# Kernel tuning notes

Hardware: AMD Instinct MI355X
Metric: run time of the kernel (lower is better)

## Reference

```python
import jax, jax.numpy as jnp
import numpy as np

MARGIN = 1.0
N, D = 8192, 128
NUM_CLASSES = 1024


def setup_inputs() -> dict:
    key = jax.random.key(0)
    k1, k2, k3 = jax.random.split(key, 3)
    a = jax.random.normal(k1, (N, D), dtype=jnp.float32)
    b = jax.random.normal(k2, (N, D), dtype=jnp.float32)
    # L2-normalize embeddings (standard for metric learning; keeps exp() stable)
    a = a / jnp.linalg.norm(a, axis=1, keepdims=True)
    b = b / jnp.linalg.norm(b, axis=1, keepdims=True)
    labels = jax.random.randint(k3, (N,), 0, NUM_CLASSES, dtype=jnp.int64 if jax.config.jax_enable_x64 else jnp.int32)
    return {"a": a, "b": b, "labels": labels}


def reference(a, b, labels):
    # S[i, j] = a_i . b_j  -- full pairwise similarity, one GEMM
    S = a @ b.T  # [N, N]
    same = labels[:, None] == labels[None, :]  # [N, N]
    eye = jnp.eye(labels.shape[0], dtype=bool)
    pos_mask = same & ~eye          # ordered positive pairs (i != j, same label)
    neg_mask = ~same                # ordered negative pairs (labels differ)
    # V[i] = sum_k in neg(i) exp(margin + S[i, k])
    V = jnp.sum(jnp.where(neg_mask, jnp.exp(MARGIN + S), 0.0), axis=1)  # [N]
    # per positive pair (i, j): max(log(V_i + V_j) - S_ij, 0)^2
    hinge = jnp.maximum(jnp.log(V[:, None] + V[None, :]) - S, 0.0)
    comp = jnp.where(pos_mask, hinge * hinge, 0.0)
    num_pos = jnp.sum(pos_mask)
    loss = jnp.sum(comp) / (2.0 * num_pos.astype(S.dtype))
    return loss
```

## Files before the change

### kernel.cpp

```cpp
#include <hip/hip_runtime.h>

#define NN 8192
#define DD 128
#define MAXCLS 64
#define NCHUNK 8
#define LOG2E 1.4426950408889634f
#define E1    2.718281828459045f

typedef __attribute__((ext_vector_type(8))) short bf16x8;
typedef __attribute__((ext_vector_type(4))) float f32x4;

#if __has_builtin(__builtin_amdgcn_exp2f)
#define EXP2F(x) __builtin_amdgcn_exp2f(x)
#else
#define EXP2F(x) exp2f(x)
#endif

__device__ __forceinline__ void load16_lds(const unsigned short* g, unsigned short* l) {
    __builtin_amdgcn_global_load_lds(
        (const __attribute__((address_space(1))) unsigned int*)g,
        (__attribute__((address_space(3))) unsigned int*)l,
        16, 0, 0);
}

__device__ __forceinline__ unsigned short f2bf(float x) {
    unsigned u = __float_as_uint(x);
    u = (u + 0x7FFFu + ((u >> 16) & 1u)) >> 16;
    return (unsigned short)u;
}

__global__ __launch_bounds__(256) void ml_convert_kernel(
    const float* __restrict__ a, const float* __restrict__ b,
    const int* __restrict__ labels,
    unsigned short* __restrict__ abf, unsigned short* __restrict__ bbf,
    int* __restrict__ cnt, int* __restrict__ list)
{
    int t = blockIdx.x * 256 + threadIdx.x;
    const float* src = a;
    unsigned short* dst = abf;
    int idx = t;
    float scale = LOG2E;
    if (t >= 262144) { src = b; dst = bbf; idx = t - 262144; scale = 1.0f; }
    float4 v = ((const float4*)src)[idx];
    ushort4 o;
    o.x = f2bf(v.x * scale); o.y = f2bf(v.y * scale);
    o.z = f2bf(v.z * scale); o.w = f2bf(v.w * scale);
    ((ushort4*)dst)[idx] = o;

    if (t < NN) {
        int c = labels[t];
        int p = atomicAdd(&cnt[c], 1);
        if (p < MAXCLS) list[c * MAXCLS + p] = t;
    }
}

__global__ __launch_bounds__(256, 2) void ml_vsum_gemm_kernel(
    const unsigned short* __restrict__ abf, const unsigned short* __restrict__ bbf,
    float* __restrict__ Vp)
{
    __shared__ unsigned short As[128 * DD];
    __shared__ unsigned short Bs[2][64 * DD];
    __shared__ float red[2][64];

    const int tid  = threadIdx.x;
    const int lane = tid & 63;
    const int wv   = tid >> 6;
    const int row0 = blockIdx.y * 128;
    const int j0   = blockIdx.x * 1024;

    const int lr = lane >> 4;
    const int sp = lane & 15;
    const int m  = lane & 15;
    const int q  = lane >> 4;
    const int xr = m & 7;

#pragma unroll
    for (int i = 0; i < 8; i++) {
        int rb = wv * 32 + i * 4;
        int r  = rb + lr;
        int cc = sp ^ (r & 7);
        load16_lds(&abf[(size_t)(row0 + r) * DD + cc * 8], &As[rb * DD]);
    }
#pragma unroll
    for (int i = 0; i < 4; i++) {
        int rb = wv * 16 + i * 4;
        int r  = rb + lr;
        int cc = sp ^ (r & 7);
        load16_lds(&bbf[(size_t)(j0 + r) * DD + cc * 8], &Bs[0][rb * DD]);
    }
#pragma unroll
    for (int i = 0; i < 4; i++) {
        int rb = wv * 16 + i * 4;
        int r  = rb + lr;
        int cc = sp ^ (r & 7);
        load16_lds(&bbf[(size_t)(j0 + 64 + r) * DD + cc * 8], &Bs[1][rb * DD]);
    }
    __syncthreads();

    const int wi = (wv >> 1) * 64;
    const int wj = (wv & 1) * 32;

    bf16x8 afr[4][4];
#pragma unroll
    for (int ti = 0; ti < 4; ti++)
#pragma unroll
        for (int ks = 0; ks < 4; ks++) {
            int r   = wi + ti * 16 + m;
            int pos = (ks * 4 + q) ^ xr;
            afr[ti][ks] = *(const bf16x8*)(&As[r * DD + pos * 8]);
        }

    float rs[4][4];
#pragma unroll
    for (int ti = 0; ti < 4; ti++)
#pragma unroll
        for (int rg = 0; rg < 4; rg++) rs[ti][rg] = 0.f;

    const f32x4 zero = {0.f, 0.f, 0.f, 0.f};

#pragma unroll 2
    for (int jt = 0; jt < 16; jt++) {
        const int pb = jt & 1;
        f32x4 acc[4][2];
#pragma unroll
        for (int ti = 0; ti < 4; ti++)
#pragma unroll
            for (int tj = 0; tj < 2; tj++) acc[ti][tj] = zero;

#pragma unroll
        for (int ks = 0; ks < 4; ks++) {
            bf16x8 bfr[2];
#pragma unroll
            for (int tj = 0; tj < 2; tj++) {
                int r   = wj + tj * 16 + m;
                int pos = (ks * 4 + q) ^ xr;
                bfr[tj] = *(const bf16x8*)(&Bs[pb][r * DD + pos * 8]);
            }
#pragma unroll
            for (int ti = 0; ti < 4; ti++)
#pragma unroll
                for (int tj = 0; tj < 2; tj++)
                    acc[ti][tj] = __builtin_amdgcn_mfma_f32_16x16x32_bf16(afr[ti][ks], bfr[tj], acc[ti][tj], 0, 0, 0);
        }

#pragma unroll
        for (int ti = 0; ti < 4; ti++)
#pragma unroll
            for (int tj = 0; tj < 2; tj++) {
                f32x4 c = acc[ti][tj];
                rs[ti][0] += EXP2F(c[0]);
                rs[ti][1] += EXP2F(c[1]);
                rs[ti][2] += EXP2F(c[2]);
                rs[ti][3] += EXP2F(c[3]);
            }

        __syncthreads();
        if (jt < 14) {
            int jb = j0 + (jt + 2) * 64;
#pragma unroll
            for (int i = 0; i < 4; i++) {
                int rb = wv * 16 + i * 4;
                int r  = rb + lr;
                int cc = sp ^ (r & 7);
                load16_lds(&bbf[(size_t)(jb + r) * DD + cc * 8], &Bs[pb][rb * DD]);
            }
        }
    }

#pragma unroll
    for (int ti = 0; ti < 4; ti++)
#pragma unroll
        for (int rg = 0; rg < 4; rg++) {
            float v = rs[ti][rg];
            v += __shfl_xor(v, 1);
            v += __shfl_xor(v, 2);
            v += __shfl_xor(v, 4);
            v += __shfl_xor(v, 8);
            rs[ti][rg] = v;
        }

    if ((wv & 1) == 1 && m == 0) {
#pragma unroll
        for (int ti = 0; ti < 4; ti++)
#pragma unroll
            for (int rg = 0; rg < 4; rg++)
                red[wv >> 1][ti * 16 + q * 4 + rg] = rs[ti][rg];
    }
    __syncthreads();
    if ((wv & 1) == 0 && m == 0) {
#pragma unroll
        for (int ti = 0; ti < 4; ti++)
#pragma unroll
            for (int rg = 0; rg < 4; rg++) {
                int rloc = ti * 16 + q * 4 + rg;
                Vp[(size_t)blockIdx.x * NN + row0 + wi + rloc] = rs[ti][rg] + red[wv >> 1][rloc];
            }
    }
}

__global__ __launch_bounds__(256) void ml_pairs_kernel(
    const float* __restrict__ a, const float* __restrict__ b,
    const int* __restrict__ cnt, const int* __restrict__ list,
    const float* __restrict__ Vp,
    float* __restrict__ classLoss, int* __restrict__ classCnt)
{
    __shared__ int   mem[MAXCLS];
    __shared__ float sumExp[MAXCLS];
    __shared__ float Vadj[MAXCLS];
    __shared__ float Sc[MAXCLS * MAXCLS];
    __shared__ float ps[4];
    __shared__ int   cs[4];

    const int c   = blockIdx.x;
    const int tid = threadIdx.x;
    int mc = cnt[c];
    if (mc > MAXCLS) mc = MAXCLS;

    float vsum = 0.f;
    if (tid < mc) {
        int r = list[c * MAXCLS + tid];
        mem[tid] = r;
#pragma unroll
        for (int jc = 0; jc < NCHUNK; jc++) vsum += Vp[(size_t)jc * NN + r];
    }
    if (tid < MAXCLS) sumExp[tid] = 0.f;
    __syncthreads();

    const int g = tid >> 4;
    const int l = tid & 15;
    const int tot1 = mc * mc;
    for (int pp = g; pp < tot1; pp += 16) {
        int i = pp / mc;
        int j = pp - i * mc;
        int ri = mem[i], rj = mem[j];
        const float4* ar = (const float4*)(a + (size_t)ri * DD) + l * 2;
        const float4* br = (const float4*)(b + (size_t)rj * DD) + l * 2;
        float4 a0 = ar[0], a1 = ar[1];
        float4 b0 = br[0], b1 = br[1];
        float s = 0.f;
        s = fmaf(a0.x, b0.x, s); s = fmaf(a0.y, b0.y, s);
        s = fmaf(a0.z, b0.z, s); s = fmaf(a0.w, b0.w, s);
        s = fmaf(a1.x, b1.x, s); s = fmaf(a1.y, b1.y, s);
        s = fmaf(a1.z, b1.z, s); s = fmaf(a1.w, b1.w, s);
        s += __shfl_xor(s, 1);
        s += __shfl_xor(s, 2);
        s += __shfl_xor(s, 4);
        s += __shfl_xor(s, 8);
        if (l == 0) {
            Sc[i * MAXCLS + j] = s;
            atomicAdd(&sumExp[i], __expf(s));
        }
    }
    __syncthreads();

    if (tid < mc) Vadj[tid] = E1 * (vsum - sumExp[tid]);
    __syncthreads();

    float partial = 0.f;
    int   count   = 0;
    for (int pp = tid; pp < tot1; pp += 256) {
        int i = pp / mc;
        int j = pp - i * mc;
        if (i != j) {
            float h = fmaxf(logf(Vadj[i] + Vadj[j]) - Sc[i * MAXCLS + j], 0.f);
            partial += h * h;
            count++;
        }
    }
    for (int off = 32; off > 0; off >>= 1) {
        partial += __shfl_down(partial, off);
        count   += __shfl_down(count, off);
    }
    const int lane = tid & 63, wv = tid >> 6;
    if (lane == 0) { ps[wv] = partial; cs[wv] = count; }
    __syncthreads();
    if (tid == 0) {
        classLoss[c] = ps[0] + ps[1] + ps[2] + ps[3];
        classCnt[c]  = cs[0] + cs[1] + cs[2] + cs[3];
    }
}

__global__ __launch_bounds__(256) void ml_finalize_kernel(
    const float* __restrict__ classLoss, const int* __restrict__ classCnt,
    float* __restrict__ out)
{
    __shared__ double dred[4];
    __shared__ long long cred[4];
    const int tid = threadIdx.x;
    const int lane = tid & 63, wv = tid >> 6;

    double dls = 0.0;
    long long dct = 0;
    for (int k = tid; k < 1024; k += 256) {
        dls += (double)classLoss[k];
        dct += (long long)classCnt[k];
    }
    for (int off = 32; off > 0; off >>= 1) {
        dls += __shfl_down(dls, off);
        dct += __shfl_down(dct, off);
    }
    if (lane == 0) { dred[wv] = dls; cred[wv] = dct; }
    __syncthreads();
    if (tid == 0) {
        double ls = dred[0] + dred[1] + dred[2] + dred[3];
        long long np = cred[0] + cred[1] + cred[2] + cred[3];
        out[0] = (float)(ls / (2.0 * (double)np));
    }
}

extern "C" void kernel_launch(void* const* d_in, const int* in_sizes, int n_in,
                              void* d_out, int out_size, void* d_ws, size_t ws_size,
                              hipStream_t stream)
{
    const float* a      = (const float*)d_in[0];
    const float* b      = (const float*)d_in[1];
    const int*   labels = (const int*)d_in[2];
    float* out = (float*)d_out;

    char* ws = (char*)d_ws;
    unsigned short* abf = (unsigned short*)ws;
    unsigned short* bbf = (unsigned short*)(ws + 2097152);
    char*     base2     = ws + 4194304;
    int*      cnt       = (int*)(base2);
    float*    classLoss = (float*)(base2 + 8192);
    int*      classCnt  = (int*)(base2 + 12288);
    int*      list      = (int*)(base2 + 16384);
    float*    Vp        = (float*)(base2 + 278528);

    (void)hipMemsetAsync(cnt, 0, 4096, stream);

    ml_convert_kernel<<<2048, 256, 0, stream>>>(a, b, labels, abf, bbf, cnt, list);

    dim3 g(NCHUNK, NN / 128);
    ml_vsum_gemm_kernel<<<g, 256, 0, stream>>>(abf, bbf, Vp);

    ml_pairs_kernel<<<1024, 256, 0, stream>>>(a, b, cnt, list, Vp, classLoss, classCnt);

    ml_finalize_kernel<<<1, 256, 0, stream>>>(classLoss, classCnt, out);
}
```

Before: 104.0 us.

## Widen B tiles to 128 columns, reuse A smem, and pipeline loads with exp epilogue

The V-sum GEMM kernel drops the separate A shared buffer and reuses its space, so there are two 128-row B buffers in the same LDS footprint. Each wave now computes a 64x64 tile per step instead of 64x32, and the j-loop runs over 8 tiles of 128 instead of 16 of 64. The loop is restructured so the next B tile's global-to-LDS load is issued before the exp2 epilogue, with explicit waitcnt/barrier control and setprio around the MFMA block. This is meant to cut the barrier count and overlap memory with compute, at the cost of more accumulator registers, which may hurt occupancy under launch_bounds(256,2). The reduction over wj after the loop may need to match the new 64-wide wave split.

```diff
diff --git a/kernel.cpp b/kernel.cpp
--- a/kernel.cpp
+++ b/kernel.cpp
@@ -58,8 +58,7 @@
     const unsigned short* __restrict__ abf, const unsigned short* __restrict__ bbf,
     float* __restrict__ Vp)
 {
-    __shared__ unsigned short As[128 * DD];
-    __shared__ unsigned short Bs[2][64 * DD];
+    __shared__ unsigned short Bs[2][128 * DD];
     __shared__ float red[2][64];
 
     const int tid  = threadIdx.x;
@@ -79,26 +78,19 @@
         int rb = wv * 32 + i * 4;
         int r  = rb + lr;
         int cc = sp ^ (r & 7);
-        load16_lds(&abf[(size_t)(row0 + r) * DD + cc * 8], &As[rb * DD]);
-    }
-#pragma unroll
-    for (int i = 0; i < 4; i++) {
-        int rb = wv * 16 + i * 4;
+        load16_lds(&abf[(size_t)(row0 + r) * DD + cc * 8], &Bs[0][rb * DD]);
+    }
+#pragma unroll
+    for (int i = 0; i < 8; i++) {
+        int rb = wv * 32 + i * 4;
         int r  = rb + lr;
         int cc = sp ^ (r & 7);
-        load16_lds(&bbf[(size_t)(j0 + r) * DD + cc * 8], &Bs[0][rb * DD]);
-    }
-#pragma unroll
-    for (int i = 0; i < 4; i++) {
-        int rb = wv * 16 + i * 4;
-        int r  = rb + lr;
-        int cc = sp ^ (r & 7);
-        load16_lds(&bbf[(size_t)(j0 + 64 + r) * DD + cc * 8], &Bs[1][rb * DD]);
+        load16_lds(&bbf[(size_t)(j0 + r) * DD + cc * 8], &Bs[1][rb * DD]);
     }
     __syncthreads();
 
     const int wi = (wv >> 1) * 64;
-    const int wj = (wv & 1) * 32;
+    const int wj = (wv & 1) * 64;
 
     bf16x8 afr[4][4];
 #pragma unroll
@@ -107,8 +99,18 @@
         for (int ks = 0; ks < 4; ks++) {
             int r   = wi + ti * 16 + m;
             int pos = (ks * 4 + q) ^ xr;
-            afr[ti][ks] = *(const bf16x8*)(&As[r * DD + pos * 8]);
-        }
+            afr[ti][ks] = *(const bf16x8*)(&Bs[0][r * DD + pos * 8]);
+        }
+    asm volatile("s_waitcnt lgkmcnt(0)" ::: "memory");
+    __syncthreads();
+
+#pragma unroll
+    for (int i = 0; i < 8; i++) {
+        int rb = wv * 32 + i * 4;
+        int r  = rb + lr;
+        int cc = sp ^ (r & 7);
+        load16_lds(&bbf[(size_t)(j0 + 128 + r) * DD + cc * 8], &Bs[0][rb * DD]);
+    }
 
     float rs[4][4];
 #pragma unroll
@@ -117,55 +119,77 @@
         for (int rg = 0; rg < 4; rg++) rs[ti][rg] = 0.f;
 
     const f32x4 zero = {0.f, 0.f, 0.f, 0.f};
+    f32x4 acc[4][4];
+
+#define COMPUTE_TILE(BUF)                                                              \
+    {                                                                                  \
+        __builtin_amdgcn_s_setprio(1);                                                 \
+        _Pragma("unroll")                                                              \
+        for (int ks = 0; ks < 4; ks++) {                                               \
+            bf16x8 bfr[4];                                                             \
+            _Pragma("unroll")                                                          \
+            for (int tj = 0; tj < 4; tj++) {                                           \
+                int r   = wj + tj * 16 + m;                                            \
+                int pos = (ks * 4 + q) ^ xr;                                           \
+                bfr[tj] = *(const bf16x8*)(&Bs[BUF][r * DD + pos * 8]);                \
+            }                                                                          \
+            _Pragma("unroll")                                                          \
+            for (int ti = 0; ti < 4; ti++)                                             \
+                _Pragma("unroll")                                                      \
+                for (int tj = 0; tj < 4; tj++)                                         \
+                    acc[ti][tj] = __builtin_amdgcn_mfma_f32_16x16x32_bf16(             \
+                        afr[ti][ks], bfr[tj], (ks == 0) ? zero : acc[ti][tj], 0, 0, 0);\
+        }                                                                              \
+        __builtin_amdgcn_s_setprio(0);                                                 \
+    }
+
+#define STAGE_B(JT, BUF)                                                               \
+    _Pragma("unroll")                                                                  \
+    for (int i = 0; i < 8; i++) {                                                      \
+        int rb = wv * 32 + i * 4;                                                      \
+        int r  = rb + lr;                                                              \
+        int cc = sp ^ (r & 7);                                                         \
+        load16_lds(&bbf[(size_t)(j0 + (JT) * 128 + r) * DD + cc * 8],                  \
+                   &Bs[BUF][rb * DD]);                                                 \
+    }
+
+#define EPILOGUE()                                                                     \
+    _Pragma("unroll")                                                                  \
+    for (int ti = 0; ti < 4; ti++)                                                     \
+        _Pragma("unroll")                                                              \
+        for (int tj = 0; tj < 4; tj++) {                                               \
+            f32x4 c = acc[ti][tj];                                                     \
+            rs[ti][0] += EXP2F(c[0]);                                                  \
+            rs[ti][1] += EXP2F(c[1]);                                                  \
+            rs[ti][2] += EXP2F(c[2]);                                                  \
+            rs[ti][3] += EXP2F(c[3]);                                                  \
+        }
 
 #pragma unroll 2
-    for (int jt = 0; jt < 16; jt++) {
-        const int pb = jt & 1;
-        f32x4 acc[4][2];
-#pragma unroll
-        for (int ti = 0; ti < 4; ti++)
-#pragma unroll
-            for (int tj = 0; tj < 2; tj++) acc[ti][tj] = zero;
-
-#pragma unroll
-        for (int ks = 0; ks < 4; ks++) {
-            bf16x8 bfr[2];
-#pragma unroll
-            for (int tj = 0; tj < 2; tj++) {
-                int r   = wj + tj * 16 + m;
-                int pos = (ks * 4 + q) ^ xr;
-                bfr[tj] = *(const bf16x8*)(&Bs[pb][r * DD + pos * 8]);
-            }
-#pragma unroll
-            for (int ti = 0; ti < 4; ti++)
-#pragma unroll
-                for (int tj = 0; tj < 2; tj++)
-                    acc[ti][tj] = __builtin_amdgcn_mfma_f32_16x16x32_bf16(afr[ti][ks], bfr[tj], acc[ti][tj], 0, 0, 0);
-        }
-
-#pragma unroll
-        for (int ti = 0; ti < 4; ti++)
-#pragma unroll
-            for (int tj = 0; tj < 2; tj++) {
-                f32x4 c = acc[ti][tj];
-                rs[ti][0] += EXP2F(c[0]);
-                rs[ti][1] += EXP2F(c[1]);
-                rs[ti][2] += EXP2F(c[2]);
-                rs[ti][3] += EXP2F(c[3]);
-            }
-
-        __syncthreads();
-        if (jt < 14) {
-            int jb = j0 + (jt + 2) * 64;
-#pragma unroll
-            for (int i = 0; i < 4; i++) {
-                int rb = wv * 16 + i * 4;
-                int r  = rb + lr;
-                int cc = sp ^ (r & 7);
-                load16_lds(&bbf[(size_t)(jb + r) * DD + cc * 8], &Bs[pb][rb * DD]);
-            }
-        }
-    }
+    for (int jt = 0; jt < 6; jt++) {
+        const int cb = (jt + 1) & 1;
+        COMPUTE_TILE(cb);
+        asm volatile("s_waitcnt lgkmcnt(0)" ::: "memory");
+        __builtin_amdgcn_s_barrier();
+        STAGE_B(jt + 2, cb);
+        EPILOGUE();
+        asm volatile("s_waitcnt vmcnt(8)" ::: "memory");
+        __builtin_amdgcn_s_barrier();
+    }
+    {
+        COMPUTE_TILE(1);
+        EPILOGUE();
+        asm volatile("s_waitcnt vmcnt(0)" ::: "memory");
+        __builtin_amdgcn_s_barrier();
+    }
+    {
+        COMPUTE_TILE(0);
+        EPILOGUE();
+    }
+
+#undef COMPUTE_TILE
+#undef STAGE_B
+#undef EPILOGUE
 
 #pragma unroll
     for (int ti = 0; ti < 4; ti++)
```

Result: no change. 103.8 us (-0.2%).
